# Optimization experiments

Hardware: AMD Instinct MI355X
Metric: run time of the kernel (lower is better)

The kernel has to match this reference:

```python
import jax, jax.numpy as jnp
import numpy as np


def _pairwise_sqdist(x, y):
    # x: [B, N, 3], y: [B, M, 3] -> [B, N, M] squared distances
    x2 = jnp.sum(x * x, axis=-1, keepdims=True)          # [B, N, 1]
    y2 = jnp.sum(y * y, axis=-1)[:, None, :]             # [B, 1, M]
    xy = jnp.einsum('bnd,bmd->bnm', x, y)                # [B, N, M]
    return jnp.maximum(x2 + y2 - 2.0 * xy, 0.0)


def _chamfer_l1(x, y):
    # PoinTr-style ChamferDistanceL1: mean sqrt NN dist both ways, averaged
    d = _pairwise_sqdist(x, y)                           # [B, N, M]
    d1 = jnp.sqrt(jnp.min(d, axis=2))                    # x -> nearest in y
    d2 = jnp.sqrt(jnp.min(d, axis=1))                    # y -> nearest in x
    return 0.5 * (jnp.mean(d1) + jnp.mean(d2))


def setup_inputs() -> dict:
    key = jax.random.key(0)
    k1, k2, k3, k4 = jax.random.split(key, 4)
    B, Nc, Nf = 4, 1024, 8192
    return {
        'ret_coarse': jax.random.normal(k1, (B, Nc, 3), dtype=jnp.float32),
        'ret_fine':   jax.random.normal(k2, (B, Nf, 3), dtype=jnp.float32),
        'gt_fine':    jax.random.normal(k3, (B, Nf, 3), dtype=jnp.float32),
        'gt_coarse':  jax.random.normal(k4, (B, Nc, 3), dtype=jnp.float32),
    }


def reference(ret_coarse, ret_fine, gt_fine, gt_coarse):
    loss_fine = _chamfer_l1(ret_fine, gt_fine)
    # coarse L2 point-distance loss: mean over (B, Nc) of per-point L2 norm
    loss_coarse = jnp.mean(jnp.sqrt(jnp.sum((ret_coarse - gt_coarse) ** 2, axis=2)))
    return (loss_coarse, loss_fine)
```

## Files before the change

### kernel.cpp

```cpp
#include <hip/hip_runtime.h>

#define B  4
#define NF 8192
#define NC 1024
#define TJ (NF / 32)
#define BANDS 128
#define TPW 32

#define NMIN (2 * B * NF)
#define NCRS (B * NC)
#define NTOT (NMIN + NCRS)

typedef _Float16 h8   __attribute__((ext_vector_type(8)));
typedef float    f16v __attribute__((ext_vector_type(16)));


__global__ __launch_bounds__(256) void k_prep(const float* __restrict__ rf,
                                              const float* __restrict__ gf,
                                              h8* __restrict__ fragbuf) {
    int id  = blockIdx.x * 256 + threadIdx.x;
    int src = id >> 16;
    int rem = id & 65535;
    int b   = rem >> 14;
    int jt  = (rem >> 6) & (TJ - 1);
    int ln  = rem & 63;
    int n   = ln & 31, kg = ln >> 5;

    const float* y = (src ? rf : gf) + ((size_t)(b * NF) + jt * 32 + n) * 3;
    float y0 = y[0], y1 = y[1], y2 = y[2];
    float t0 = -2.0f * y0, t1 = -2.0f * y1, t2 = -2.0f * y2;
    _Float16 mh0 = (_Float16)t0, mh1 = (_Float16)t1, mh2 = (_Float16)t2;
    _Float16 ml0 = (_Float16)(t0 - (float)mh0);
    _Float16 ml1 = (_Float16)(t1 - (float)mh1);
    _Float16 ml2 = (_Float16)(t2 - (float)mh2);
    float sy = fmaf(y0, y0, fmaf(y1, y1, y2 * y2));
    _Float16 syh = (_Float16)sy;
    _Float16 syl = (_Float16)(sy - (float)syh);

    h8 fr = {};
    if (kg == 0) {
        fr[0] = mh0; fr[1] = mh1; fr[2] = mh2;
        fr[3] = mh0; fr[4] = mh1; fr[5] = mh2;
        fr[6] = ml0; fr[7] = ml1;
    } else {
        fr[0] = ml2; fr[1] = (_Float16)1.0f; fr[2] = (_Float16)1.0f;
        fr[3] = syh; fr[4] = syl;
    }
    fragbuf[((size_t)(src * B + b) * TJ + jt) * 64 + ln] = fr;
}

__global__ __launch_bounds__(512) void k_main(const float* __restrict__ rf,
                                              const float* __restrict__ gf,
                                              const h8* __restrict__ fragbuf,
                                              float* __restrict__ rowbuf) {
    __shared__ float rbuf[8][64];

    int bx   = blockIdx.x;
    int dir  = bx >> 9;
    int rem  = bx & 511;
    int b    = rem >> 7;
    int band = rem & 127;
    int t  = threadIdx.x;
    int ln = t & 63, w = t >> 6, m = ln & 31, kg = ln >> 5;

    const float* xp = dir ? gf : rf;
    h8 afr[2];
#pragma unroll
    for (int f = 0; f < 2; ++f) {
        const float* xr = xp + ((size_t)(b * NF) + band * 64 + f * 32 + m) * 3;
        float x0 = xr[0], x1 = xr[1], x2 = xr[2];
        _Float16 h0 = (_Float16)x0, h1 = (_Float16)x1, h2 = (_Float16)x2;
        _Float16 l0 = (_Float16)(x0 - (float)h0);
        _Float16 l1 = (_Float16)(x1 - (float)h1);
        _Float16 l2 = (_Float16)(x2 - (float)h2);
        float sx = fmaf(x0, x0, fmaf(x1, x1, x2 * x2));
        _Float16 sh = (_Float16)sx;
        _Float16 sl = (_Float16)(sx - (float)sh);
        h8 fr = {};
        if (kg == 0) {
            fr[0] = h0; fr[1] = h1; fr[2] = h2;
            fr[3] = l0; fr[4] = l1; fr[5] = l2;
            fr[6] = h0; fr[7] = h1;
        } else {
            fr[0] = h2; fr[1] = sh; fr[2] = sl;
            fr[3] = (_Float16)1.0f; fr[4] = (_Float16)1.0f;
        }
        afr[f] = fr;
    }

    float rmin0[16], rmin1[16];
#pragma unroll
    for (int r = 0; r < 16; ++r) { rmin0[r] = 3.4e38f; rmin1[r] = 3.4e38f; }

    const h8* p = fragbuf + ((size_t)(dir * B + b) * TJ + w * TPW) * 64 + ln;
    h8 b0 = p[0];
    h8 b1 = p[64];
#pragma unroll 2
    for (int q = 0; q < TPW / 2; ++q) {
        h8 n0 = p[(2 * q + 2) * 64];
        h8 n1 = p[(2 * q + 3) * 64];
        f16v c00 = __builtin_amdgcn_mfma_f32_32x32x16_f16(afr[0], b0, (f16v){}, 0, 0, 0);
        f16v c01 = __builtin_amdgcn_mfma_f32_32x32x16_f16(afr[0], b1, (f16v){}, 0, 0, 0);
#pragma unroll
        for (int r = 0; r < 16; ++r)
            rmin0[r] = fminf(fminf(c00[r], c01[r]), rmin0[r]);
        f16v c10 = __builtin_amdgcn_mfma_f32_32x32x16_f16(afr[1], b0, (f16v){}, 0, 0, 0);
        f16v c11 = __builtin_amdgcn_mfma_f32_32x32x16_f16(afr[1], b1, (f16v){}, 0, 0, 0);
#pragma unroll
        for (int r = 0; r < 16; ++r)
            rmin1[r] = fminf(fminf(c10[r], c11[r]), rmin1[r]);
        b0 = n0;
        b1 = n1;
    }

#pragma unroll
    for (int off = 1; off <= 16; off <<= 1) {
#pragma unroll
        for (int r = 0; r < 16; ++r) {
            rmin0[r] = fminf(rmin0[r], __shfl_xor(rmin0[r], off));
            rmin1[r] = fminf(rmin1[r], __shfl_xor(rmin1[r], off));
        }
    }
    if (m == 0) {
#pragma unroll
        for (int r = 0; r < 16; ++r) {
            int row = 4 * kg + (r & 3) + 8 * (r >> 2);
            rbuf[w][row]      = rmin0[r];
            rbuf[w][32 + row] = rmin1[r];
        }
    }
    __syncthreads();
    if (t < 64) {
        float v = rbuf[0][t];
#pragma unroll
        for (int ww = 1; ww < 8; ++ww) v = fminf(v, rbuf[ww][t]);
        rowbuf[(size_t)dir * (B * NF) + b * NF + band * 64 + t] =
            sqrtf(fmaxf(v, 0.0f));
    }
}

__global__ __launch_bounds__(256) void k_reduce(const float* __restrict__ rowbuf,
                                                const float* __restrict__ rc,
                                                const float* __restrict__ gc,
                                                float* __restrict__ out) {
    float s_crs = 0.f, s_fine = 0.f;
    for (int i = blockIdx.x * 256 + threadIdx.x; i < NTOT; i += gridDim.x * 256) {
        if (i < NMIN) {
            s_fine += rowbuf[i];
        } else {
            int pnt = i - NMIN;
            float dx = rc[3 * pnt + 0] - gc[3 * pnt + 0];
            float dy = rc[3 * pnt + 1] - gc[3 * pnt + 1];
            float dz = rc[3 * pnt + 2] - gc[3 * pnt + 2];
            s_crs += sqrtf(fmaf(dx, dx, fmaf(dy, dy, dz * dz)));
        }
    }
#pragma unroll
    for (int off = 32; off > 0; off >>= 1) {
        s_crs  += __shfl_down(s_crs, off);
        s_fine += __shfl_down(s_fine, off);
    }
    __shared__ float red[2][4];
    int lane = threadIdx.x & 63, w = threadIdx.x >> 6;
    if (lane == 0) { red[0][w] = s_crs; red[1][w] = s_fine; }
    __syncthreads();
    if (threadIdx.x == 0) {
        float t0 = red[0][0] + red[0][1] + red[0][2] + red[0][3];
        float t1 = red[1][0] + red[1][1] + red[1][2] + red[1][3];
        atomicAdd(&out[0], t0 * (1.0f / (float)NCRS));
        atomicAdd(&out[1], t1 * (0.5f / (float)(B * NF)));
    }
}

extern "C" void kernel_launch(void* const* d_in, const int* in_sizes, int n_in,
                              void* d_out, int out_size, void* d_ws, size_t ws_size,
                              hipStream_t stream) {
    const float* rc = (const float*)d_in[0];
    const float* rf = (const float*)d_in[1];
    const float* gf = (const float*)d_in[2];
    const float* gc = (const float*)d_in[3];

    float* rowbuf  = (float*)d_ws;
    h8*    fragbuf = (h8*)((char*)d_ws + (size_t)NMIN * 4);
    float* out     = (float*)d_out;

    hipMemsetAsync(out, 0, 2 * sizeof(float), stream);
    k_prep<<<512, 256, 0, stream>>>(rf, gf, fragbuf);
    k_main<<<2 * B * BANDS, 512, 0, stream>>>(rf, gf, fragbuf, rowbuf);
    k_reduce<<<64, 256, 0, stream>>>(rowbuf, rc, gc, out);
}
```

Baseline: 97.01 us.

## Swap MFMA operand roles, fuse reductions into prep and main kernels

Query points now sit on the MFMA B (column) side and the target fragments stream in as the A operand, so each lane's per-column minimum reduces mostly inside registers and needs only one cross-half shuffle instead of a five-step butterfly. Each block now covers 128 query points, which reduces the register-resident min state. The separate reduce kernel and its rowbuf round trip are removed: the coarse loss is folded into k_prep and the fine loss is accumulated by atomics at the end of k_main. The cost is more atomic traffic on out[1] and a different grid ordering that interleaves batch and direction across blocks.

```diff
diff --git a/kernel.cpp b/kernel.cpp
--- a/kernel.cpp
+++ b/kernel.cpp
@@ -4,12 +4,10 @@
 #define NF 8192
 #define NC 1024
 #define TJ (NF / 32)
-#define BANDS 128
-#define TPW 32
+#define TPW (TJ / 8)
+#define XT 128
 
-#define NMIN (2 * B * NF)
 #define NCRS (B * NC)
-#define NTOT (NMIN + NCRS)
 
 typedef _Float16 h8   __attribute__((ext_vector_type(8)));
 typedef float    f16v __attribute__((ext_vector_type(16)));
@@ -17,7 +15,10 @@
 
 __global__ __launch_bounds__(256) void k_prep(const float* __restrict__ rf,
                                               const float* __restrict__ gf,
-                                              h8* __restrict__ fragbuf) {
+                                              h8* __restrict__ fragbuf,
+                                              const float* __restrict__ rc,
+                                              const float* __restrict__ gc,
+                                              float* __restrict__ out) {
     int id  = blockIdx.x * 256 + threadIdx.x;
     int src = id >> 16;
     int rem = id & 65535;
@@ -28,147 +29,120 @@
 
     const float* y = (src ? rf : gf) + ((size_t)(b * NF) + jt * 32 + n) * 3;
     float y0 = y[0], y1 = y[1], y2 = y[2];
-    float t0 = -2.0f * y0, t1 = -2.0f * y1, t2 = -2.0f * y2;
-    _Float16 mh0 = (_Float16)t0, mh1 = (_Float16)t1, mh2 = (_Float16)t2;
-    _Float16 ml0 = (_Float16)(t0 - (float)mh0);
-    _Float16 ml1 = (_Float16)(t1 - (float)mh1);
-    _Float16 ml2 = (_Float16)(t2 - (float)mh2);
+    _Float16 h0 = (_Float16)y0, h1 = (_Float16)y1, h2 = (_Float16)y2;
+    _Float16 l0 = (_Float16)(y0 - (float)h0);
+    _Float16 l1 = (_Float16)(y1 - (float)h1);
+    _Float16 l2 = (_Float16)(y2 - (float)h2);
     float sy = fmaf(y0, y0, fmaf(y1, y1, y2 * y2));
-    _Float16 syh = (_Float16)sy;
-    _Float16 syl = (_Float16)(sy - (float)syh);
+    _Float16 sh = (_Float16)sy;
+    _Float16 sl = (_Float16)(sy - (float)sh);
 
     h8 fr = {};
     if (kg == 0) {
-        fr[0] = mh0; fr[1] = mh1; fr[2] = mh2;
-        fr[3] = mh0; fr[4] = mh1; fr[5] = mh2;
-        fr[6] = ml0; fr[7] = ml1;
+        fr[0] = h0; fr[1] = h1; fr[2] = h2;
+        fr[3] = l0; fr[4] = l1; fr[5] = l2;
+        fr[6] = h0; fr[7] = h1;
     } else {
-        fr[0] = ml2; fr[1] = (_Float16)1.0f; fr[2] = (_Float16)1.0f;
-        fr[3] = syh; fr[4] = syl;
+        fr[0] = h2; fr[1] = sh; fr[2] = sl;
+        fr[3] = (_Float16)1.0f; fr[4] = (_Float16)1.0f;
     }
     fragbuf[((size_t)(src * B + b) * TJ + jt) * 64 + ln] = fr;
+
+    if (id < NCRS) {
+        float dx = rc[3 * id + 0] - gc[3 * id + 0];
+        float dy = rc[3 * id + 1] - gc[3 * id + 1];
+        float dz = rc[3 * id + 2] - gc[3 * id + 2];
+        float s = sqrtf(fmaf(dx, dx, fmaf(dy, dy, dz * dz)));
+#pragma unroll
+        for (int off = 32; off > 0; off >>= 1) s += __shfl_down(s, off);
+        if ((threadIdx.x & 63) == 0)
+            atomicAdd(&out[0], s * (1.0f / (float)NCRS));
+    }
 }
 
 __global__ __launch_bounds__(512) void k_main(const float* __restrict__ rf,
                                               const float* __restrict__ gf,
                                               const h8* __restrict__ fragbuf,
-                                              float* __restrict__ rowbuf) {
-    __shared__ float rbuf[8][64];
+                                              float* __restrict__ out) {
+    __shared__ float rbuf[8][XT];
 
-    int bx   = blockIdx.x;
-    int dir  = bx >> 9;
-    int rem  = bx & 511;
-    int b    = rem >> 7;
-    int band = rem & 127;
-    int t  = threadIdx.x;
+    int bx  = blockIdx.x;
+    int reg = bx & 7;
+    int dir = reg >> 2;
+    int b   = reg & 3;
+    int xg  = bx >> 3;
+    int t   = threadIdx.x;
     int ln = t & 63, w = t >> 6, m = ln & 31, kg = ln >> 5;
 
     const float* xp = dir ? gf : rf;
-    h8 afr[2];
+    h8 bfr[4];
 #pragma unroll
-    for (int f = 0; f < 2; ++f) {
-        const float* xr = xp + ((size_t)(b * NF) + band * 64 + f * 32 + m) * 3;
+    for (int f = 0; f < 4; ++f) {
+        const float* xr = xp + ((size_t)(b * NF) + xg * XT + f * 32 + m) * 3;
         float x0 = xr[0], x1 = xr[1], x2 = xr[2];
-        _Float16 h0 = (_Float16)x0, h1 = (_Float16)x1, h2 = (_Float16)x2;
-        _Float16 l0 = (_Float16)(x0 - (float)h0);
-        _Float16 l1 = (_Float16)(x1 - (float)h1);
-        _Float16 l2 = (_Float16)(x2 - (float)h2);
+        float t0 = -2.0f * x0, t1 = -2.0f * x1, t2 = -2.0f * x2;
+        _Float16 mh0 = (_Float16)t0, mh1 = (_Float16)t1, mh2 = (_Float16)t2;
+        _Float16 ml0 = (_Float16)(t0 - (float)mh0);
+        _Float16 ml1 = (_Float16)(t1 - (float)mh1);
+        _Float16 ml2 = (_Float16)(t2 - (float)mh2);
         float sx = fmaf(x0, x0, fmaf(x1, x1, x2 * x2));
         _Float16 sh = (_Float16)sx;
         _Float16 sl = (_Float16)(sx - (float)sh);
         h8 fr = {};
         if (kg == 0) {
-            fr[0] = h0; fr[1] = h1; fr[2] = h2;
-            fr[3] = l0; fr[4] = l1; fr[5] = l2;
-            fr[6] = h0; fr[7] = h1;
+            fr[0] = mh0; fr[1] = mh1; fr[2] = mh2;
+            fr[3] = mh0; fr[4] = mh1; fr[5] = mh2;
+            fr[6] = ml0; fr[7] = ml1;
         } else {
-            fr[0] = h2; fr[1] = sh; fr[2] = sl;
-            fr[3] = (_Float16)1.0f; fr[4] = (_Float16)1.0f;
+            fr[0] = ml2; fr[1] = (_Float16)1.0f; fr[2] = (_Float16)1.0f;
+            fr[3] = sh;  fr[4] = sl;
         }
-        afr[f] = fr;
+        bfr[f] = fr;
     }
 
-    float rmin0[16], rmin1[16];
+    float mn[4];
 #pragma unroll
-    for (int r = 0; r < 16; ++r) { rmin0[r] = 3.4e38f; rmin1[r] = 3.4e38f; }
+    for (int f = 0; f < 4; ++f) mn[f] = 3.4e38f;
 
     const h8* p = fragbuf + ((size_t)(dir * B + b) * TJ + w * TPW) * 64 + ln;
-    h8 b0 = p[0];
-    h8 b1 = p[64];
+    h8 a0 = p[0];
+    h8 a1 = p[64];
 #pragma unroll 2
     for (int q = 0; q < TPW / 2; ++q) {
         h8 n0 = p[(2 * q + 2) * 64];
         h8 n1 = p[(2 * q + 3) * 64];
-        f16v c00 = __builtin_amdgcn_mfma_f32_32x32x16_f16(afr[0], b0, (f16v){}, 0, 0, 0);
-        f16v c01 = __builtin_amdgcn_mfma_f32_32x32x16_f16(afr[0], b1, (f16v){}, 0, 0, 0);
 #pragma unroll
-        for (int r = 0; r < 16; ++r)
-            rmin0[r] = fminf(fminf(c00[r], c01[r]), rmin0[r]);
-        f16v c10 = __builtin_amdgcn_mfma_f32_32x32x16_f16(afr[1], b0, (f16v){}, 0, 0, 0);
-        f16v c11 = __builtin_amdgcn_mfma_f32_32x32x16_f16(afr[1], b1, (f16v){}, 0, 0, 0);
+        for (int f = 0; f < 4; ++f) {
+            f16v c0 = __builtin_amdgcn_mfma_f32_32x32x16_f16(a0, bfr[f], (f16v){}, 0, 0, 0);
+            f16v c1 = __builtin_amdgcn_mfma_f32_32x32x16_f16(a1, bfr[f], (f16v){}, 0, 0, 0);
+            float pa = fminf(c0[0], c1[0]);
+            float pb = fminf(c0[1], c1[1]);
 #pragma unroll
-        for (int r = 0; r < 16; ++r)
-            rmin1[r] = fminf(fminf(c10[r], c11[r]), rmin1[r]);
-        b0 = n0;
-        b1 = n1;
+            for (int r = 2; r < 16; r += 2) {
+                pa = fminf(fminf(c0[r], c1[r]), pa);
+                pb = fminf(fminf(c0[r + 1], c1[r + 1]), pb);
+            }
+            mn[f] = fminf(fminf(pa, pb), mn[f]);
+        }
+        a0 = n0;
+        a1 = n1;
     }
 
 #pragma unroll
-    for (int off = 1; off <= 16; off <<= 1) {
-#pragma unroll
-        for (int r = 0; r < 16; ++r) {
-            rmin0[r] = fminf(rmin0[r], __shfl_xor(rmin0[r], off));
-            rmin1[r] = fminf(rmin1[r], __shfl_xor(rmin1[r], off));
-        }
-    }
-    if (m == 0) {
-#pragma unroll
-        for (int r = 0; r < 16; ++r) {
-            int row = 4 * kg + (r & 3) + 8 * (r >> 2);
-            rbuf[w][row]      = rmin0[r];
-            rbuf[w][32 + row] = rmin1[r];
-        }
+    for (int f = 0; f < 4; ++f) {
+        float v = fminf(mn[f], __shfl_xor(mn[f], 32));
+        if (kg == 0) rbuf[w][f * 32 + m] = v;
     }
     __syncthreads();
-    if (t < 64) {
+    if (t < XT) {
         float v = rbuf[0][t];
 #pragma unroll
         for (int ww = 1; ww < 8; ++ww) v = fminf(v, rbuf[ww][t]);
-        rowbuf[(size_t)dir * (B * NF) + b * NF + band * 64 + t] =
-            sqrtf(fmaxf(v, 0.0f));
-    }
-}
-
-__global__ __launch_bounds__(256) void k_reduce(const float* __restrict__ rowbuf,
-                                                const float* __restrict__ rc,
-                                                const float* __restrict__ gc,
-                                                float* __restrict__ out) {
-    float s_crs = 0.f, s_fine = 0.f;
-    for (int i = blockIdx.x * 256 + threadIdx.x; i < NTOT; i += gridDim.x * 256) {
-        if (i < NMIN) {
-            s_fine += rowbuf[i];
-        } else {
-            int pnt = i - NMIN;
-            float dx = rc[3 * pnt + 0] - gc[3 * pnt + 0];
-            float dy = rc[3 * pnt + 1] - gc[3 * pnt + 1];
-            float dz = rc[3 * pnt + 2] - gc[3 * pnt + 2];
-            s_crs += sqrtf(fmaf(dx, dx, fmaf(dy, dy, dz * dz)));
-        }
-    }
+        float s = sqrtf(fmaxf(v, 0.0f));
 #pragma unroll
-    for (int off = 32; off > 0; off >>= 1) {
-        s_crs  += __shfl_down(s_crs, off);
-        s_fine += __shfl_down(s_fine, off);
-    }
-    __shared__ float red[2][4];
-    int lane = threadIdx.x & 63, w = threadIdx.x >> 6;
-    if (lane == 0) { red[0][w] = s_crs; red[1][w] = s_fine; }
-    __syncthreads();
-    if (threadIdx.x == 0) {
-        float t0 = red[0][0] + red[0][1] + red[0][2] + red[0][3];
-        float t1 = red[1][0] + red[1][1] + red[1][2] + red[1][3];
-        atomicAdd(&out[0], t0 * (1.0f / (float)NCRS));
-        atomicAdd(&out[1], t1 * (0.5f / (float)(B * NF)));
+        for (int off = 32; off > 0; off >>= 1) s += __shfl_down(s, off);
+        if ((t & 63) == 0)
+            atomicAdd(&out[1], s * (0.5f / (float)(B * NF)));
     }
 }
 
@@ -180,12 +154,10 @@
     const float* gf = (const float*)d_in[2];
     const float* gc = (const float*)d_in[3];
 
-    float* rowbuf  = (float*)d_ws;
-    h8*    fragbuf = (h8*)((char*)d_ws + (size_t)NMIN * 4);
+    h8*    fragbuf = (h8*)d_ws;
     float* out     = (float*)d_out;
 
     hipMemsetAsync(out, 0, 2 * sizeof(float), stream);
-    k_prep<<<512, 256, 0, stream>>>(rf, gf, fragbuf);
-    k_main<<<2 * B * BANDS, 512, 0, stream>>>(rf, gf, fragbuf, rowbuf);
-    k_reduce<<<64, 256, 0, stream>>>(rowbuf, rc, gc, out);
+    k_prep<<<512, 256, 0, stream>>>(rf, gf, fragbuf, rc, gc, out);
+    k_main<<<512, 512, 0, stream>>>(rf, gf, fragbuf, out);
 }
```

New measurement: 87.13 us. 10.2% less time.
